# Kernel optimization log

Measured on AMD Instinct MI355X. Metric: run time of the kernel, lower is better.

The kernel has to match this reference:

```python
import jax, jax.numpy as jnp
import numpy as np

EMBED = 1024
HEADS = 16
HEAD_DIM = EMBED // HEADS


def setup_inputs() -> dict:
    key = jax.random.key(0)
    kx, kq, kk, kv, ko = jax.random.split(key, 5)
    s = 1.0 / np.sqrt(EMBED)
    return {
        "x": jax.random.normal(kx, (4, 2048, EMBED), dtype=jnp.float32),
        "Wq": jax.random.uniform(kq, (EMBED, EMBED), jnp.float32, -s, s),
        "Wk": jax.random.uniform(kk, (EMBED, EMBED), jnp.float32, -s, s),
        "Wv": jax.random.uniform(kv, (EMBED, EMBED), jnp.float32, -s, s),
        "Wo": jax.random.uniform(ko, (EMBED, EMBED), jnp.float32, -s, s),
    }


def reference(x, Wq, Wk, Wv, Wo):
    B, S, E = x.shape
    # nn.Linear computes x @ W.T; weights stored as (out, in)
    q = (x @ Wq.T).reshape(B, S, HEADS, HEAD_DIM).transpose(0, 2, 1, 3)  # [B,H,S,D]
    k = (x @ Wk.T).reshape(B, S, HEADS, HEAD_DIM).transpose(0, 2, 1, 3)
    v = (x @ Wv.T).reshape(B, S, HEADS, HEAD_DIM).transpose(0, 2, 1, 3)
    scores = jnp.einsum("bhsd,bhtd->bhst", q, k) / np.sqrt(HEAD_DIM)  # [B,H,S,S]
    causal = jnp.triu(jnp.ones((S, S), dtype=bool), k=1)
    scores = jnp.where(causal[None, None], -jnp.inf, scores)
    probs = jax.nn.softmax(scores, axis=-1)  # dropout_rate=0 -> identity
    attn = jnp.einsum("bhst,bhtd->bhsd", probs, v)  # [B,H,S,D]
    attn = attn.transpose(0, 2, 1, 3).reshape(B, S, E)
    return attn @ Wo.T
```

## Files before the change

### kernel.cpp

```cpp
#include <hip/hip_runtime.h>

#define EMB 1024
#define NHEADS 16
#define HD 64
#define BATCH 4
#define SEQ 2048
#define MTOK (BATCH*SEQ)

typedef __bf16 bf16x8 __attribute__((ext_vector_type(8)));
typedef __bf16 bf16x4 __attribute__((ext_vector_type(4)));
typedef float  f32x4  __attribute__((ext_vector_type(4)));

#define MFMA16(a,b,c) __builtin_amdgcn_mfma_f32_16x16x32_bf16(a,b,c,0,0,0)

__device__ __forceinline__ void gload_lds16(const __bf16* g, __bf16* l) {
    __builtin_amdgcn_global_load_lds(
        (__attribute__((address_space(1))) void*)(g),
        (__attribute__((address_space(3))) void*)(l), 16, 0, 0);
}

__global__ void cvt_all(const float* __restrict__ x,  const float* __restrict__ wq,
                        const float* __restrict__ wk, const float* __restrict__ wv,
                        const float* __restrict__ wo,
                        __bf16* xb, __bf16* wqb, __bf16* wkb, __bf16* wvb, __bf16* wob) {
    int bid = blockIdx.x;
    int z, rel;
    if (bid < 8192) { z = 0; rel = bid; }
    else            { z = 1 + ((bid - 8192) >> 10); rel = (bid - 8192) & 1023; }
    const float* src = (z == 0) ? x : (z == 1) ? wq : (z == 2) ? wk : (z == 3) ? wv : wo;
    __bf16*      dst = (z == 0) ? xb : (z == 1) ? wqb : (z == 2) ? wkb : (z == 3) ? wvb : wob;
    int i = (rel * 256 + threadIdx.x) * 4;
    float4 v = *(const float4*)(src + i);
    bf16x4 o = { (__bf16)v.x, (__bf16)v.y, (__bf16)v.z, (__bf16)v.w };
    *(bf16x4*)(dst + i) = o;
}

__global__ __launch_bounds__(256) void transpose_v(const __bf16* __restrict__ vb,
                                                   __bf16* __restrict__ vt) {
    __shared__ __bf16 t[64 * 72];
    const int tid = threadIdx.x;
    const int bh = blockIdx.y, s0 = blockIdx.x * 64;
    const __bf16* src = vb + ((size_t)bh * SEQ + s0) * HD;
    int sr = tid >> 3, cc = (tid & 7) * 8;
    bf16x8 a0 = *(const bf16x8*)(src + (size_t)sr * HD + cc);
    bf16x8 a1 = *(const bf16x8*)(src + (size_t)(sr + 32) * HD + cc);
    *(bf16x8*)(t + sr * 72 + cc)        = a0;
    *(bf16x8*)(t + (sr + 32) * 72 + cc) = a1;
    __syncthreads();
    int dr = tid >> 3, g = tid & 7;
    __bf16* dstb = vt + (size_t)bh * HD * SEQ + s0;
    #pragma unroll
    for (int it = 0; it < 2; ++it) {
        int d = dr + it * 32;
        bf16x8 o;
        #pragma unroll
        for (int j = 0; j < 8; ++j) o[j] = t[(g * 8 + j) * 72 + d];
        *(bf16x8*)(dstb + (size_t)d * SEQ + g * 8) = o;
    }
}

#define SCHEDB() __builtin_amdgcn_sched_barrier(0)
#define PH_MID_LG(n)                                                    \
    do { SCHEDB(); __builtin_amdgcn_s_barrier();                        \
         asm volatile("s_waitcnt lgkmcnt(" #n ")" ::: "memory");        \
         SCHEDB(); __builtin_amdgcn_s_setprio(1); } while (0)
#define PH_END()                                                        \
    do { __builtin_amdgcn_s_setprio(0); SCHEDB();                       \
         __builtin_amdgcn_s_barrier(); SCHEDB(); } while (0)
#define PH_END_VM0()                                                    \
    do { __builtin_amdgcn_s_setprio(0); SCHEDB();                       \
         asm volatile("s_waitcnt vmcnt(0)" ::: "memory");               \
         __builtin_amdgcn_s_barrier(); SCHEDB(); } while (0)
#define PH_END_VM2()                                                    \
    do { __builtin_amdgcn_s_setprio(0); SCHEDB();                       \
         asm volatile("s_waitcnt vmcnt(2)" ::: "memory");               \
         __builtin_amdgcn_s_barrier(); SCHEDB(); } while (0)

#define MM_N01(AF, G)                                                   \
    do { _Pragma("unroll") for (int m_ = 0; m_ < 4; ++m_) {             \
         _Pragma("unroll") for (int n_ = 0; n_ < 2; ++n_) {             \
            f32x4 c_ = acc[(G)*4 + m_][n_];                             \
            c_ = MFMA16(AF[m_][0], bfA[n_][0], c_);                     \
            c_ = MFMA16(AF[m_][1], bfA[n_][1], c_);                     \
            acc[(G)*4 + m_][n_] = c_; } } } while (0)

#define MM_N2()                                                         \
    do { _Pragma("unroll") for (int m_ = 0; m_ < 4; ++m_) {             \
            f32x4 c_ = acc[m_][2];                                      \
            c_ = MFMA16(afA[m_][0], bfB[0], c_);                        \
            c_ = MFMA16(afA[m_][1], bfB[1], c_);                        \
            acc[m_][2] = c_;                                            \
            f32x4 d_ = acc[4 + m_][2];                                  \
            d_ = MFMA16(afB[m_][0], bfB[0], d_);                        \
            d_ = MFMA16(afB[m_][1], bfB[1], d_);                        \
            acc[4 + m_][2] = d_; } } while (0)

__device__ __forceinline__ void gemm6ph192(
    const __bf16* __restrict__ Ag,
    const __bf16* __restrict__ Bg,
    __bf16* __restrict__ As, __bf16* __restrict__ Bs,
    f32x4 (&acc)[8][3])
{
    const int tid   = threadIdx.x;
    const int w     = tid >> 6;
    const int mlane = tid & 15;
    const int quad  = (tid >> 4) & 3;
    const int wm    = w >> 2;
    const int wn    = w & 3;

    const int e0  = (quad ^ (mlane & 7)) * 8;
    const int aB0 = (wn * 48 + mlane) * 64 + e0;
    const int aB2 = (wn * 48 + 32 + mlane) * 64 + e0;

    const int so = (tid >> 3) * 1024 + (((tid & 7) ^ ((tid >> 3) & 7)) * 8);
    const int sd = (tid & ~63) * 8;

    const auto stA1 = [&](int slot, int c, int kt) {
        gload_lds16(Ag + c * 65536 + kt + so, As + slot * 16384 + c * 4096 + sd);
    };
    const auto stB1 = [&](int slot, int c, int kt) {
        gload_lds16(Bg + c * 65536 + kt + so, Bs + slot * 12288 + c * 4096 + sd);
    };
    const auto rdA2 = [&](bf16x8 (&dst)[4][2], int slot, int grp) {
        const __bf16* base = As + slot * 16384 + wm * 8192 + grp * 4096;
        const int o0 = mlane * 64 + e0;
        #pragma unroll
        for (int m = 0; m < 4; ++m) {
            dst[m][0] = *(const bf16x8*)(base + m * 1024 + o0);
            dst[m][1] = *(const bf16x8*)(base + m * 1024 + (o0 ^ 32));
        }
    };
    const auto rdB01 = [&](bf16x8 (&dst)[2][2], int slot) {
        const __bf16* base = Bs + slot * 12288;
        #pragma unroll
        for (int n = 0; n < 2; ++n) {
            dst[n][0] = *(const bf16x8*)(base + n * 1024 + aB0);
            dst[n][1] = *(const bf16x8*)(base + n * 1024 + (aB0 ^ 32));
        }
    };
    const auto rdB2 = [&](bf16x8 (&dst)[2], int slot) {
        const __bf16* base = Bs + slot * 12288;
        dst[0] = *(const bf16x8*)(base + aB2);
        dst[1] = *(const bf16x8*)(base + (aB2 ^ 32));
    };

    const f32x4 fz = {0.f, 0.f, 0.f, 0.f};
    #pragma unroll
    for (int i = 0; i < 8; ++i)
        #pragma unroll
        for (int j = 0; j < 3; ++j) acc[i][j] = fz;

    bf16x8 afA[4][2], afB[4][2], bfA[2][2], bfB[2];

    stA1(0, 0, 0); stA1(0, 1, 0); stA1(0, 2, 0); stA1(0, 3, 0);
    stB1(0, 0, 0); stB1(0, 1, 0); stB1(0, 2, 0);
    stA1(1, 0, 64); stA1(1, 1, 64);
    asm volatile("s_waitcnt vmcnt(2)" ::: "memory");
    SCHEDB(); __builtin_amdgcn_s_barrier(); SCHEDB();

    #pragma unroll 1
    for (int t = 0; t < 8; ++t) {
        const bool last = (t == 7);
        const int k_s1 = t * 128 + 64;
        const int k_n0 = t * 128 + 128;
        const int k_n1 = t * 128 + 192;

        SCHEDB();
        rdA2(afA, 0, 0); rdB01(bfA, 0);
        SCHEDB();
        rdA2(afB, 0, 1);
        SCHEDB();
        rdB2(bfB, 0);
        SCHEDB();
        stA1(1, 2, k_s1); stA1(1, 3, k_s1);
        PH_MID_LG(10); MM_N01(afA, 0); PH_END();

        stB1(1, 0, k_s1); stB1(1, 1, k_s1);
        PH_MID_LG(2); MM_N01(afB, 1); PH_END();

        stB1(1, 2, k_s1);
        if (!last) { stA1(0, 0, k_n0); stA1(0, 1, k_n0); }
        PH_MID_LG(0); MM_N2();
        if (last) PH_END_VM0(); else PH_END_VM2();

        SCHEDB();
        rdA2(afA, 1, 0); rdB01(bfA, 1);
        SCHEDB();
        rdA2(afB, 1, 1);
        SCHEDB();
        rdB2(bfB, 1);
        SCHEDB();
        if (!last) { stA1(0, 2, k_n0); stA1(0, 3, k_n0); }
        PH_MID_LG(10); MM_N01(afA, 0); PH_END();

        if (!last) { stB1(0, 0, k_n0); stB1(0, 1, k_n0); }
        PH_MID_LG(2); MM_N01(afB, 1); PH_END();

        if (!last) { stB1(0, 2, k_n0); stA1(1, 0, k_n1); stA1(1, 1, k_n1); }
        PH_MID_LG(0); MM_N2();
        if (last) PH_END(); else PH_END_VM2();
    }
}

__global__ __launch_bounds__(512, 2) void qkv_gemm(
    const __bf16* __restrict__ xb, const __bf16* __restrict__ wqkv,
    __bf16* __restrict__ Qb, __bf16* __restrict__ Kb, __bf16* __restrict__ Vb)
{
    __shared__ __bf16 As[2 * 256 * 64];
    __shared__ __bf16 Bs[2 * 192 * 64];

    const int bid   = blockIdx.x;
    const int local = bid >> 3;
    const int mt    = (bid & 7) * 4 + (local & 3);
    const int nt    = local >> 2;

    f32x4 acc[8][3];
    gemm6ph192(xb + (size_t)mt * 262144, wqkv + (size_t)nt * 196608, As, Bs, acc);

    const int tid = threadIdx.x, w = tid >> 6;
    const int mlane = tid & 15, quad = (tid >> 4) & 3;
    const int wm = w >> 2, wn = w & 3;
    const int rowb = mt * 256 + wm * 128;
    const int colb = nt * 192 + wn * 48;

    #pragma unroll
    for (int ni = 0; ni < 3; ++ni) {
        int gcol = colb + ni * 16 + mlane;
        int z = gcol >> 10, cc = gcol & 1023;
        int h = cc >> 6, d = cc & 63;
        __bf16* O = (z == 0) ? Qb : (z == 1) ? Kb : Vb;
        float scl = (z == 0) ? 0.18033688011112042f : 1.0f;
        #pragma unroll
        for (int mi = 0; mi < 8; ++mi) {
            int grow = rowb + (mi >> 2) * 64 + (mi & 3) * 16 + quad * 4;
            int b = grow >> 11, s = grow & 2047;
            #pragma unroll
            for (int r = 0; r < 4; ++r)
                O[(((size_t)b * NHEADS + h) * SEQ + (s + r)) * HD + d] =
                    (__bf16)(acc[mi][ni][r] * scl);
        }
    }
}

#define MMAQ(AF, BF, MH, NHI)                                           \
    do {                                                                \
        _Pragma("unroll")                                               \
        for (int m_ = 0; m_ < 4; ++m_) {                                \
            f32x4 c_ = acc[(MH)*4 + m_][(NHI)];                         \
            c_ = MFMA16(AF[m_][0], BF[0][0], c_);                       \
            c_ = MFMA16(AF[m_][1], BF[0][1], c_);                       \
            acc[(MH)*4 + m_][(NHI)] = c_;                               \
        }                                                               \
    } while (0)

__device__ __forceinline__ void gemm8ph128(
    const __bf16* __restrict__ Ag,
    const __bf16* __restrict__ Bg,
    __bf16* __restrict__ As, __bf16* __restrict__ Bs,
    f32x4 (&acc)[8][2])
{
    const int tid   = threadIdx.x;
    const int w     = tid >> 6;
    const int mlane = tid & 15;
    const int quad  = (tid >> 4) & 3;
    const int wm    = w >> 2;
    const int wn    = w & 3;

    const int e0  = (quad ^ (mlane & 7)) * 8;
    const int aA0 = mlane * 64 + e0;
    const int aB0 = (wn * 32 + mlane) * 64 + e0;

    const int so = (tid >> 3) * 1024 + (((tid & 7) ^ ((tid >> 3) & 7)) * 8);
    const int sd = (tid & ~63) * 8;

    const auto stA = [&](int slot, int half, int kt) {
        const __bf16* g = Ag + half * 131072 + kt + so;
        __bf16* l = As + slot * 16384 + half * 8192 + sd;
        gload_lds16(g, l);
        gload_lds16(g + 65536, l + 4096);
    };
    const auto stB = [&](int slot, int kt) {
        const __bf16* g = Bg + kt + so;
        __bf16* l = Bs + slot * 8192 + sd;
        gload_lds16(g, l);
        gload_lds16(g + 65536, l + 4096);
    };
    const auto rdA = [&](bf16x8 (&dst)[4][2], int slot, int grp) {
        const __bf16* base = As + slot * 16384 + wm * 8192 + grp * 4096;
        #pragma unroll
        for (int m = 0; m < 4; ++m) {
            dst[m][0] = *(const bf16x8*)(base + m * 1024 + aA0);
            dst[m][1] = *(const bf16x8*)(base + m * 1024 + (aA0 ^ 32));
        }
    };
    const auto rdB = [&](bf16x8 (&dst)[1][2], int slot, int nh) {
        const __bf16* base = Bs + slot * 8192 + nh * 1024;
        dst[0][0] = *(const bf16x8*)(base + aB0);
        dst[0][1] = *(const bf16x8*)(base + (aB0 ^ 32));
    };

    const f32x4 fz = {0.f, 0.f, 0.f, 0.f};
    #pragma unroll
    for (int i = 0; i < 8; ++i)
        #pragma unroll
        for (int j = 0; j < 2; ++j) acc[i][j] = fz;

    bf16x8 afA[4][2], afB[4][2], bfA[1][2], bfB[1][2];

    stA(0, 0, 0); stA(0, 1, 0); stB(0, 0);
    stA(1, 0, 64);
    asm volatile("s_waitcnt vmcnt(2)" ::: "memory");
    SCHEDB(); __builtin_amdgcn_s_barrier(); SCHEDB();

    #pragma unroll 1
    for (int t = 0; t < 8; ++t) {
        const bool last = (t == 7);
        const int ktc1 = t * 128 + 64;
        const int ktn0 = t * 128 + 128;
        const int ktn1 = t * 128 + 192;

        SCHEDB();
        rdA(afA, 0, 0); rdB(bfA, 0, 0);
        SCHEDB();
        rdA(afB, 0, 1);
        SCHEDB();
        rdB(bfB, 0, 1);
        SCHEDB();
        stA(1, 1, ktc1);
        PH_MID_LG(10); MMAQ(afA, bfA, 0, 0); PH_END();

        stB(1, ktc1);
        PH_MID_LG(2); MMAQ(afB, bfA, 1, 0); PH_END();

        PH_MID_LG(0); MMAQ(afA, bfB, 0, 1); PH_END();

        if (!last) stA(0, 0, ktn0);
        PH_MID_LG(0); MMAQ(afB, bfB, 1, 1);
        if (last) PH_END_VM0(); else PH_END_VM2();

        SCHEDB();
        rdA(afA, 1, 0); rdB(bfA, 1, 0);
        SCHEDB();
        rdA(afB, 1, 1);
        SCHEDB();
        rdB(bfB, 1, 1);
        SCHEDB();
        if (!last) stA(0, 1, ktn0);
        PH_MID_LG(10); MMAQ(afA, bfA, 0, 0); PH_END();

        if (!last) stB(0, ktn0);
        PH_MID_LG(2); MMAQ(afB, bfA, 1, 0); PH_END();

        PH_MID_LG(0); MMAQ(afA, bfB, 0, 1); PH_END();

        if (!last) stA(1, 0, ktn1);
        PH_MID_LG(0); MMAQ(afB, bfB, 1, 1);
        if (last) PH_END(); else PH_END_VM2();
    }
}

__global__ __launch_bounds__(512, 2) void out_gemm(
    const __bf16* __restrict__ attnb, const __bf16* __restrict__ wo,
    float* __restrict__ out)
{
    __shared__ __bf16 As[2 * 256 * 64];
    __shared__ __bf16 Bs[2 * 128 * 64];

    const int bid   = blockIdx.x;
    const int local = bid >> 3;
    const int mt    = (bid & 7) * 4 + (local & 3);
    const int nt    = local >> 2;

    f32x4 acc[8][2];
    gemm8ph128(attnb + (size_t)mt * 262144, wo + (size_t)nt * 131072, As, Bs, acc);

    const int tid = threadIdx.x, w = tid >> 6;
    const int mlane = tid & 15, quad = (tid >> 4) & 3;
    const int wm = w >> 2, wn = w & 3;
    const int rowb = mt * 256 + wm * 128;
    const int colb = nt * 128 + wn * 32;

    #pragma unroll
    for (int mi = 0; mi < 8; ++mi) {
        int grow = rowb + (mi >> 2) * 64 + (mi & 3) * 16 + quad * 4;
        #pragma unroll
        for (int r = 0; r < 4; ++r) {
            #pragma unroll
            for (int ni = 0; ni < 2; ++ni) {
                int gcol = colb + ni * 16 + mlane;
                out[(size_t)(grow + r) * EMB + gcol] = acc[mi][ni][r];
            }
        }
    }
}

__global__ __launch_bounds__(512, 1) void attn_kernel(
    const __bf16* __restrict__ Qb, const __bf16* __restrict__ Kb,
    const __bf16* __restrict__ Vtg, __bf16* __restrict__ attnb)
{
    __shared__ __bf16 Ks[2 * 64 * 64];
    __shared__ __bf16 Vs[2 * 64 * 64];
    __shared__ __bf16 Ps[8 * 16 * 72];

    const int tid = threadIdx.x, w = tid >> 6, lane = tid & 63;
    const int mlane = lane & 15, quad = lane >> 4;
    const int h = blockIdx.y, b = blockIdx.z;
    const size_t headoff = ((size_t)b * NHEADS + h) * SEQ * HD;
    const __bf16* Qg = Qb + headoff;
    const __bf16* Kg = Kb + headoff;
    const __bf16* Vg = Vtg + headoff;
    __bf16* Psw = Ps + w * 16 * 72;
    const int g0 = quad ^ (mlane & 7);
    const f32x4 fzero = {0.f, 0.f, 0.f, 0.f};

    const int st_row = tid >> 3;
    const int st_cc  = (tid & 7) ^ (st_row & 7);
    const int st_dst = (tid & ~63) * 8;

    for (int sp = 0; sp < 2; ++sp) {
        const int strip = sp ? (15 - (int)blockIdx.x) : (int)blockIdx.x;
        const int qw  = strip * 128 + w * 16;
        const int nch = 2 * strip + 2;

        __syncthreads();

        gload_lds16(Kg + (size_t)st_row * HD + st_cc * 8, Ks + st_dst);
        gload_lds16(Vg + (size_t)st_row * SEQ + st_cc * 8, Vs + st_dst);

        bf16x8 bq0 = *(const bf16x8*)(Qg + (size_t)(qw + mlane) * HD + quad * 8);
        bf16x8 bq1 = *(const bf16x8*)(Qg + (size_t)(qw + mlane) * HD + 32 + quad * 8);

        float l_acc = 0.f;
        f32x4 o[4];
        #pragma unroll
        for (int dt = 0; dt < 4; ++dt) o[dt] = fzero;

        for (int c = 0; c < nch; ++c) {
            const int tb = c * 64;
            const __bf16* Kp = Ks + (c & 1) * 4096;
            const __bf16* Vp = Vs + (c & 1) * 4096;
            __bf16* Kn = Ks + ((c & 1) ^ 1) * 4096;
            __bf16* Vn = Vs + ((c & 1) ^ 1) * 4096;

            asm volatile("s_waitcnt vmcnt(0)" ::: "memory");
            __syncthreads();

            if (c + 1 < nch) {
                const int tbn = tb + 64;
                gload_lds16(Kg + (size_t)(tbn + st_row) * HD + st_cc * 8, Kn + st_dst);
                gload_lds16(Vg + (size_t)st_row * SEQ + tbn + st_cc * 8, Vn + st_dst);
            }

            const int rel = qw + 15 - tb;
            if (rel >= 0) {
                f32x4 s[4];
                #pragma unroll
                for (int mt = 0; mt < 4; ++mt) {
                    const __bf16* ka = Kp + (mt * 16 + mlane) * 64;
                    bf16x8 ak0 = *(const bf16x8*)(ka + g0 * 8);
                    bf16x8 ak1 = *(const bf16x8*)(ka + (g0 ^ 4) * 8);
                    s[mt] = MFMA16(ak1, bq1, MFMA16(ak0, bq0, fzero));
                }
                if (rel < 78) {
                    const int qrel = qw + mlane - tb - quad * 4;
                    #pragma unroll
                    for (int mt = 0; mt < 4; ++mt)
                        #pragma unroll
                        for (int r = 0; r < 4; ++r)
                            if (mt * 16 + r > qrel) s[mt][r] = -3e38f;
                }

                f32x4 vsum = fzero;
                #pragma unroll
                for (int mt = 0; mt < 4; ++mt) {
                    #pragma unroll
                    for (int r = 0; r < 4; ++r)
                        s[mt][r] = __builtin_amdgcn_exp2f(s[mt][r]);
                    vsum += s[mt];
                    bf16x4 pb = { (__bf16)s[mt][0], (__bf16)s[mt][1],
                                  (__bf16)s[mt][2], (__bf16)s[mt][3] };
                    *(bf16x4*)(Psw + mlane * 72 + mt * 16 + quad * 4) = pb;
                }
                l_acc += (vsum[0] + vsum[1]) + (vsum[2] + vsum[3]);

                #pragma unroll
                for (int ks = 0; ks < 2; ++ks) {
                    bf16x8 ap = *(const bf16x8*)(Psw + mlane * 72 + ks * 32 + quad * 8);
                    #pragma unroll
                    for (int dt = 0; dt < 4; ++dt) {
                        const __bf16* va = Vp + (dt * 16 + mlane) * 64;
                        bf16x8 bv = *(const bf16x8*)(va + (((ks * 4 + quad) ^ (mlane & 7)) * 8));
                        o[dt] = MFMA16(ap, bv, o[dt]);
                    }
                }
            }
        }

        float lf = l_acc;
        lf += __shfl_xor(lf, 16);
        lf += __shfl_xor(lf, 32);
        #pragma unroll
        for (int r = 0; r < 4; ++r) {
            float lr = __shfl(lf, quad * 4 + r);
            float linv = 1.0f / lr;
            int q = qw + quad * 4 + r;
            size_t rowoff = ((size_t)b * SEQ + q) * EMB + h * HD;
            #pragma unroll
            for (int dt = 0; dt < 4; ++dt)
                attnb[rowoff + dt * 16 + mlane] = (__bf16)(o[dt][r] * linv);
        }
    }
}

extern "C" void kernel_launch(void* const* d_in, const int* in_sizes, int n_in,
                              void* d_out, int out_size, void* d_ws, size_t ws_size,
                              hipStream_t stream) {
    const float* x  = (const float*)d_in[0];
    const float* Wq = (const float*)d_in[1];
    const float* Wk = (const float*)d_in[2];
    const float* Wv = (const float*)d_in[3];
    const float* Wo = (const float*)d_in[4];
    float* out = (float*)d_out;

    char* ws = (char*)d_ws;
    __bf16* xb    = (__bf16*)(ws);
    __bf16* wqb   = (__bf16*)(ws + 16777216);
    __bf16* wkb   = (__bf16*)(ws + 18874368);
    __bf16* wvb   = (__bf16*)(ws + 20971520);
    __bf16* wob   = (__bf16*)(ws + 23068672);
    __bf16* qb    = (__bf16*)(ws + 25165824);
    __bf16* kb    = (__bf16*)(ws + 41943040);
    __bf16* vb    = (__bf16*)(ws + 58720256);
    __bf16* attnb = (__bf16*)(ws + 75497472);
    __bf16* vtb   = xb;

    cvt_all<<<dim3(12288), 256, 0, stream>>>(x, Wq, Wk, Wv, Wo, xb, wqb, wkb, wvb, wob);

    qkv_gemm<<<dim3(512), 512, 0, stream>>>(xb, wqb, qb, kb, vb);

    transpose_v<<<dim3(SEQ / 64, BATCH * NHEADS), 256, 0, stream>>>(vb, vtb);

    attn_kernel<<<dim3(8, NHEADS, BATCH), 512, 0, stream>>>(qb, kb, vtb, attnb);

    out_gemm<<<dim3(256), 512, 0, stream>>>(attnb, wob, out);
}
```

Measured before the change: 239.8 us.

## Process 32 query rows per wave in attention to double K/V tile reuse

Each wave now computes two 16-row query sub-tiles against every K/V chunk loaded into shared memory, so a block covers 256 query rows and the grid shrinks from 8 to 4 strips per head. The goal is to halve K/V staging traffic and shared-memory reads of K and V per MFMA. The causal strip pairing for load balance is kept. In exchange, each wave holds twice the accumulators and Q fragments, so register pressure rises. The grid also falls to 256 blocks, which lowers occupancy and the ability to hide latency.

```diff
diff --git a/kernel.cpp b/kernel.cpp
--- a/kernel.cpp
+++ b/kernel.cpp
@@ -400,7 +400,7 @@
 {
     __shared__ __bf16 Ks[2 * 64 * 64];
     __shared__ __bf16 Vs[2 * 64 * 64];
-    __shared__ __bf16 Ps[8 * 16 * 72];
+    __shared__ __bf16 Ps[8 * 32 * 72];
 
     const int tid = threadIdx.x, w = tid >> 6, lane = tid & 63;
     const int mlane = lane & 15, quad = lane >> 4;
@@ -409,7 +409,7 @@
     const __bf16* Qg = Qb + headoff;
     const __bf16* Kg = Kb + headoff;
     const __bf16* Vg = Vtg + headoff;
-    __bf16* Psw = Ps + w * 16 * 72;
+    __bf16* Psw = Ps + w * 32 * 72;
     const int g0 = quad ^ (mlane & 7);
     const f32x4 fzero = {0.f, 0.f, 0.f, 0.f};
 
@@ -418,22 +418,29 @@
     const int st_dst = (tid & ~63) * 8;
 
     for (int sp = 0; sp < 2; ++sp) {
-        const int strip = sp ? (15 - (int)blockIdx.x) : (int)blockIdx.x;
-        const int qw  = strip * 128 + w * 16;
-        const int nch = 2 * strip + 2;
+        const int strip = sp ? (7 - (int)blockIdx.x) : (int)blockIdx.x;
+        const int qw  = strip * 256 + w * 32;
+        const int nch = 4 * strip + 4;
 
         __syncthreads();
 
         gload_lds16(Kg + (size_t)st_row * HD + st_cc * 8, Ks + st_dst);
         gload_lds16(Vg + (size_t)st_row * SEQ + st_cc * 8, Vs + st_dst);
 
-        bf16x8 bq0 = *(const bf16x8*)(Qg + (size_t)(qw + mlane) * HD + quad * 8);
-        bf16x8 bq1 = *(const bf16x8*)(Qg + (size_t)(qw + mlane) * HD + 32 + quad * 8);
-
-        float l_acc = 0.f;
-        f32x4 o[4];
-        #pragma unroll
-        for (int dt = 0; dt < 4; ++dt) o[dt] = fzero;
+        bf16x8 bq[2][2];
+        #pragma unroll
+        for (int qh = 0; qh < 2; ++qh) {
+            const __bf16* qp = Qg + (size_t)(qw + qh * 16 + mlane) * HD;
+            bq[qh][0] = *(const bf16x8*)(qp + quad * 8);
+            bq[qh][1] = *(const bf16x8*)(qp + 32 + quad * 8);
+        }
+
+        float l_acc[2] = {0.f, 0.f};
+        f32x4 o[2][4];
+        #pragma unroll
+        for (int qh = 0; qh < 2; ++qh)
+            #pragma unroll
+            for (int dt = 0; dt < 4; ++dt) o[qh][dt] = fzero;
 
         for (int c = 0; c < nch; ++c) {
             const int tb = c * 64;
@@ -451,63 +458,75 @@
                 gload_lds16(Vg + (size_t)st_row * SEQ + tbn + st_cc * 8, Vn + st_dst);
             }
 
-            const int rel = qw + 15 - tb;
+            const int rel = qw + 31 - tb;
             if (rel >= 0) {
-                f32x4 s[4];
+                f32x4 s[2][4];
                 #pragma unroll
                 for (int mt = 0; mt < 4; ++mt) {
                     const __bf16* ka = Kp + (mt * 16 + mlane) * 64;
                     bf16x8 ak0 = *(const bf16x8*)(ka + g0 * 8);
                     bf16x8 ak1 = *(const bf16x8*)(ka + (g0 ^ 4) * 8);
-                    s[mt] = MFMA16(ak1, bq1, MFMA16(ak0, bq0, fzero));
+                    s[0][mt] = MFMA16(ak1, bq[0][1], MFMA16(ak0, bq[0][0], fzero));
+                    s[1][mt] = MFMA16(ak1, bq[1][1], MFMA16(ak0, bq[1][0], fzero));
                 }
-                if (rel < 78) {
-                    const int qrel = qw + mlane - tb - quad * 4;
+                if (rel < 94) {
                     #pragma unroll
-                    for (int mt = 0; mt < 4; ++mt)
+                    for (int qh = 0; qh < 2; ++qh) {
+                        const int qrel = qw + qh * 16 + mlane - tb - quad * 4;
+                        #pragma unroll
+                        for (int mt = 0; mt < 4; ++mt)
+                            #pragma unroll
+                            for (int r = 0; r < 4; ++r)
+                                if (mt * 16 + r > qrel) s[qh][mt][r] = -3e38f;
+                    }
+                }
+
+                #pragma unroll
+                for (int qh = 0; qh < 2; ++qh) {
+                    f32x4 vsum = fzero;
+                    #pragma unroll
+                    for (int mt = 0; mt < 4; ++mt) {
                         #pragma unroll
                         for (int r = 0; r < 4; ++r)
-                            if (mt * 16 + r > qrel) s[mt][r] = -3e38f;
+                            s[qh][mt][r] = __builtin_amdgcn_exp2f(s[qh][mt][r]);
+                        vsum += s[qh][mt];
+                        bf16x4 pb = { (__bf16)s[qh][mt][0], (__bf16)s[qh][mt][1],
+                                      (__bf16)s[qh][mt][2], (__bf16)s[qh][mt][3] };
+                        *(bf16x4*)(Psw + qh * 1152 + mlane * 72 + mt * 16 + quad * 4) = pb;
+                    }
+                    l_acc[qh] += (vsum[0] + vsum[1]) + (vsum[2] + vsum[3]);
                 }
-
-                f32x4 vsum = fzero;
-                #pragma unroll
-                for (int mt = 0; mt < 4; ++mt) {
-                    #pragma unroll
-                    for (int r = 0; r < 4; ++r)
-                        s[mt][r] = __builtin_amdgcn_exp2f(s[mt][r]);
-                    vsum += s[mt];
-                    bf16x4 pb = { (__bf16)s[mt][0], (__bf16)s[mt][1],
-                                  (__bf16)s[mt][2], (__bf16)s[mt][3] };
-                    *(bf16x4*)(Psw + mlane * 72 + mt * 16 + quad * 4) = pb;
-                }
-                l_acc += (vsum[0] + vsum[1]) + (vsum[2] + vsum[3]);
 
                 #pragma unroll
                 for (int ks = 0; ks < 2; ++ks) {
-                    bf16x8 ap = *(const bf16x8*)(Psw + mlane * 72 + ks * 32 + quad * 8);
+                    bf16x8 ap0 = *(const bf16x8*)(Psw + mlane * 72 + ks * 32 + quad * 8);
+                    bf16x8 ap1 = *(const bf16x8*)(Psw + 1152 + mlane * 72 + ks * 32 + quad * 8);
                     #pragma unroll
                     for (int dt = 0; dt < 4; ++dt) {
                         const __bf16* va = Vp + (dt * 16 + mlane) * 64;
                         bf16x8 bv = *(const bf16x8*)(va + (((ks * 4 + quad) ^ (mlane & 7)) * 8));
-                        o[dt] = MFMA16(ap, bv, o[dt]);
+                        o[0][dt] = MFMA16(ap0, bv, o[0][dt]);
+                        o[1][dt] = MFMA16(ap1, bv, o[1][dt]);
                     }
                 }
             }
         }
 
-        float lf = l_acc;
-        lf += __shfl_xor(lf, 16);
-        lf += __shfl_xor(lf, 32);
-        #pragma unroll
-        for (int r = 0; r < 4; ++r) {
-            float lr = __shfl(lf, quad * 4 + r);
-            float linv = 1.0f / lr;
-            int q = qw + quad * 4 + r;
-            size_t rowoff = ((size_t)b * SEQ + q) * EMB + h * HD;
+        #pragma unroll
+        for (int qh = 0; qh < 2; ++qh) {
+            float lf = l_acc[qh];
+            lf += __shfl_xor(lf, 16);
+            lf += __shfl_xor(lf, 32);
             #pragma unroll
-            for (int dt = 0; dt < 4; ++dt)
-                attnb[rowoff + dt * 16 + mlane] = (__bf16)(o[dt][r] * linv);
+            for (int r = 0; r < 4; ++r) {
+                float lr = __shfl(lf, quad * 4 + r);
+                float linv = 1.0f / lr;
+                int q = qw + qh * 16 + quad * 4 + r;
+                size_t rowoff = ((size_t)b * SEQ + q) * EMB + h * HD;
+                #pragma unroll
+                for (int dt = 0; dt < 4; ++dt)
+                    attnb[rowoff + dt * 16 + mlane] = (__bf16)(o[qh][dt][r] * linv);
+            }
         }
     }
 }
@@ -540,7 +559,7 @@
 
     transpose_v<<<dim3(SEQ / 64, BATCH * NHEADS), 256, 0, stream>>>(vb, vtb);
 
-    attn_kernel<<<dim3(8, NHEADS, BATCH), 512, 0, stream>>>(qb, kb, vtb, attnb);
+    attn_kernel<<<dim3(4, NHEADS, BATCH), 512, 0, stream>>>(qb, kb, vtb, attnb);
 
     out_gemm<<<dim3(256), 512, 0, stream>>>(attnb, wob, out);
 }
```

After: 250.7 us. +4.6%, slower.
